# Optimization experiments

Hardware: AMD Instinct MI355X
Metric: run time of the kernel (lower is better)

## Reference

```python
import jax, jax.numpy as jnp
import numpy as np

S, T, B = 50, 50, 64
SRC_V, TRG_V = 36616, 23262
E, EH, DH = 300, 512, 1024


def setup_inputs() -> dict:
    key = jax.random.key(0)
    ks = jax.random.split(key, 20)
    n = lambda k, shape: jax.random.normal(k, shape, jnp.float32) * 0.05
    return {
        "train_src_batch": jax.random.randint(ks[0], (S, B), 0, SRC_V),
        "train_trg_batch": jax.random.randint(ks[1], (T, B), 0, TRG_V),
        "emb_en": n(ks[2], (SRC_V, E)),
        "emb_de": n(ks[3], (TRG_V, E)),
        "enc_W_ih_f": n(ks[4], (4 * EH, E)),
        "enc_W_hh_f": n(ks[5], (4 * EH, EH)),
        "enc_b_f": n(ks[6], (4 * EH,)),
        "enc_W_ih_b": n(ks[7], (4 * EH, E)),
        "enc_W_hh_b": n(ks[8], (4 * EH, EH)),
        "enc_b_b": n(ks[9], (4 * EH,)),
        "dec_W_ih": n(ks[10], (4 * DH, E + DH)),
        "dec_W_hh": n(ks[11], (4 * DH, DH)),
        "dec_b": n(ks[12], (4 * DH,)),
        "W_gen": n(ks[13], (TRG_V, DH)),
        "b_gen": n(ks[14], (TRG_V,)),
        "W_i": n(ks[15], (DH, DH)),
        "W_o": n(ks[16], (DH, 2 * DH)),
    }


def _lstm_step(x, h, c, W_ih, W_hh, b):
    # PyTorch gate order: i, f, g, o
    gates = x @ W_ih.T + h @ W_hh.T + b
    i, f, g, o = jnp.split(gates, 4, axis=-1)
    c_new = jax.nn.sigmoid(f) * c + jax.nn.sigmoid(i) * jnp.tanh(g)
    h_new = jax.nn.sigmoid(o) * jnp.tanh(c_new)
    return h_new, c_new


def _run_lstm(x_seq, W_ih, W_hh, b, hidden):
    h0 = jnp.zeros((x_seq.shape[1], hidden), x_seq.dtype)
    def step(carry, x):
        h, c = carry
        h, c = _lstm_step(x, h, c, W_ih, W_hh, b)
        return (h, c), h
    (h, c), hs = jax.lax.scan(step, (h0, h0), x_seq)
    return hs, h, c


def _forward(train_src_batch, train_trg_batch, emb_en, emb_de,
             enc_W_ih_f, enc_W_hh_f, enc_b_f, enc_W_ih_b, enc_W_hh_b, enc_b_b,
             dec_W_ih, dec_W_hh, dec_b, W_gen, b_gen, W_i, W_o):
    x = emb_en[train_src_batch]                       # [S,B,E]
    hs_f, hf, cf = _run_lstm(x, enc_W_ih_f, enc_W_hh_f, enc_b_f, EH)
    hs_b, hb, cb = _run_lstm(x[::-1], enc_W_ih_b, enc_W_hh_b, enc_b_b, EH)
    output_hs = jnp.concatenate([hs_f, hs_b[::-1]], axis=-1)  # [S,B,1024]
    # Faithful to h.contiguous().view(B,1024) on direction-major [2,B,512]
    h = jnp.reshape(jnp.stack([hf, hb], axis=0), (B, DH))
    c = jnp.reshape(jnp.stack([cf, cb], axis=0), (B, DH))

    emb_trg = emb_de[train_trg_batch[: T - 1]]        # [T-1,B,E]

    def step(carry, e):
        h, c = carry
        # score[j,b] = output_hs[j,b] . (W_i h[b])  (the diag of the original mm)
        scores = jnp.einsum('sbd,bd->sb', output_hs, h @ W_i.T)
        # legacy nn.Softmax() on 2D input -> softmax over dim=1 (batch axis)
        a = jax.nn.softmax(scores, axis=1)
        s_t = jnp.einsum('sb,sbd->bd', a, output_hs)
        c_t = jnp.tanh(jnp.concatenate([s_t, h], axis=1) @ W_o.T)
        dec_in = jnp.concatenate([c_t, e], axis=1)    # [B, 1024+300]
        h, c = _lstm_step(dec_in, h, c, dec_W_ih, dec_W_hh, dec_b)
        logp = jax.nn.log_softmax(h @ W_gen.T + b_gen, axis=1)
        return (h, c), logp

    _, outs = jax.lax.scan(step, (h, c), emb_trg)     # [T-1,B,V]
    out0 = jnp.zeros((1, B, TRG_V), outs.dtype)       # output[0] filled with 0
    return jnp.concatenate([out0, outs], axis=0)      # [T,B,V]


def reference(train_src_batch, train_trg_batch, emb_en, emb_de,
              enc_W_ih_f, enc_W_hh_f, enc_b_f, enc_W_ih_b, enc_W_hh_b, enc_b_b,
              dec_W_ih, dec_W_hh, dec_b, W_gen, b_gen, W_i, W_o):
    return _forward(train_src_batch, train_trg_batch, emb_en, emb_de,
                    enc_W_ih_f, enc_W_hh_f, enc_b_f, enc_W_ih_b, enc_W_hh_b, enc_b_b,
                    dec_W_ih, dec_W_hh, dec_b, W_gen, b_gen, W_i, W_o)
```

## Files before the change

kernel.cpp:

```cpp
#include <hip/hip_runtime.h>
#include <hip/hip_bf16.h>

#define SS 50
#define TT 50
#define BB 64
#define TRGV 23262
#define EE 300
#define EH 512
#define DH 1024

#define GMRE 3136
#define GMP 3200
#define GK 1024
#define GNRE TRGV
#define GNP 23296

typedef short bf16x8 __attribute__((ext_vector_type(8)));
typedef float f32x4 __attribute__((ext_vector_type(4)));

__device__ __forceinline__ void glds16(const void* g, void* l) {
  __builtin_amdgcn_global_load_lds(
      (const __attribute__((address_space(1))) void*)g,
      (__attribute__((address_space(3))) void*)l, 16, 0, 0);
}

__device__ __forceinline__ float sigm(float x) { return 1.f / (1.f + expf(-x)); }
__device__ __forceinline__ float sum4(f32x4 v) { return v[0] + v[1] + v[2] + v[3]; }
__device__ __forceinline__ float bfu2f(unsigned short u) {
  unsigned int x = ((unsigned)u) << 16;
  return __uint_as_float(x);
}

__device__ __forceinline__ void split2(float x, __hip_bfloat16& hi, __hip_bfloat16& lo) {
  hi = __float2bfloat16(x);
  lo = __float2bfloat16(x - __bfloat162float(hi));
}

__device__ __forceinline__ void gbarg(unsigned* arrive, unsigned* gen,
                                      int idxInGrp, int n, bool poller) {
  __syncthreads();
  unsigned g = __hip_atomic_load(gen, __ATOMIC_RELAXED, __HIP_MEMORY_SCOPE_AGENT);
  if (threadIdx.x == 0)
    __hip_atomic_store(arrive + idxInGrp * 16, g + 1u, __ATOMIC_RELEASE, __HIP_MEMORY_SCOPE_AGENT);
  if (poller) {
    int i = threadIdx.x;
    if (i < n) {
      while (__hip_atomic_load(arrive + i * 16, __ATOMIC_RELAXED, __HIP_MEMORY_SCOPE_AGENT) < g + 1u)
        __builtin_amdgcn_s_sleep(1);
      (void)__hip_atomic_load(arrive + i * 16, __ATOMIC_ACQUIRE, __HIP_MEMORY_SCOPE_AGENT);
    }
    __syncthreads();
    if (threadIdx.x == 0)
      __hip_atomic_store(gen, g + 1u, __ATOMIC_RELEASE, __HIP_MEMORY_SCOPE_AGENT);
  }
  if (threadIdx.x == 0) {
    while (__hip_atomic_load(gen, __ATOMIC_RELAXED, __HIP_MEMORY_SCOPE_AGENT) < g + 1u)
      __builtin_amdgcn_s_sleep(1);
    (void)__hip_atomic_load(gen, __ATOMIC_ACQUIRE, __HIP_MEMORY_SCOPE_AGENT);
  }
  __syncthreads();
}

__global__ void k_zero(float* __restrict__ p, long n) {
  long i = (long)blockIdx.x * 256 + threadIdx.x;
  if (i < n) p[i] = 0.f;
}
__global__ void k_zero_bf(__hip_bfloat16* __restrict__ p, long n) {
  long i = (long)blockIdx.x * 256 + threadIdx.x;
  if (i < n) p[i] = __float2bfloat16(0.f);
}

__global__ void k_embed(const int* __restrict__ src, const float* __restrict__ emb,
                        float* __restrict__ x) {
  int id = blockIdx.x * 256 + threadIdx.x;
  if (id >= SS * BB * EE) return;
  int sb = id / EE, e = id % EE;
  x[id] = emb[(long)src[sb] * EE + e];
}

__global__ void k_dbperm(const float* __restrict__ db, float* __restrict__ dbp) {
  int id = blockIdx.x * 256 + threadIdx.x;
  if (id >= 4096) return;
  int u = id >> 2, g = id & 3;
  dbp[id] = db[g * 1024 + u];
}

__global__ void k_split_pad(const float* __restrict__ in, int ld_in, int col_off,
                            int Kreal, int Kpad, int rows_real, long rows_pad,
                            int mode, __hip_bfloat16* __restrict__ out) {
  long id = (long)blockIdx.x * 256 + threadIdx.x;
  if (id >= rows_pad * Kpad) return;
  long r = id / Kpad;
  int k = id % Kpad;
  float v = 0.f;
  if (r < rows_real && k < Kreal) {
    if (mode == 3) {
      v = in[(long)k * ld_in + col_off + r];
    } else {
      long sr = r;
      if (mode == 1) sr = ((49 - (r >> 6)) << 6) + (r & 63);
      else if (mode == 2) sr = (long)(r & 3) * 1024 + (r >> 2);
      v = in[sr * ld_in + col_off + k];
    }
  }
  __hip_bfloat16 hi, lo;
  split2(v, hi, lo);
  out[r * 2 * Kpad + k] = hi;
  out[r * 2 * Kpad + Kpad + k] = lo;
}

__global__ void k_embgather_split(const int* __restrict__ trg, const float* __restrict__ emb,
                                  __hip_bfloat16* __restrict__ out) {
  long id = (long)blockIdx.x * 256 + threadIdx.x;
  if (id >= 3200L * 320) return;
  long r = id / 320;
  int k = id % 320;
  int t = r >> 6, b = r & 63;
  float v = 0.f;
  if (t < TT - 1 && k < EE) v = emb[(long)trg[t * BB + b] * EE + k];
  __hip_bfloat16 hi, lo;
  split2(v, hi, lo);
  out[r * 640 + k] = hi;
  out[r * 640 + 320 + k] = lo;
}

__global__ void k_tobf16_pad(const float* __restrict__ W, __hip_bfloat16* __restrict__ Wb,
                             long nrow_real, long nrow_pad, int K) {
  long id = (long)blockIdx.x * 256 + threadIdx.x;
  if (id >= nrow_pad * K) return;
  long r = id / K;
  Wb[id] = __float2bfloat16(r < nrow_real ? W[id] : 0.f);
}

__global__ void k_repackT(const float* __restrict__ in, __hip_bfloat16* __restrict__ out) {
  long id = (long)blockIdx.x * 256 + threadIdx.x;
  if (id >= 3200L * 1024) return;
  long r = id >> 10;
  int n = id & 1023;
  out[((long)(n >> 2) * 3200 + r) * 4 + (n & 3)] = __float2bfloat16(in[id]);
}

template<int OUTBF>
__global__ __launch_bounds__(256) void k_gsplit(
    const __hip_bfloat16* __restrict__ A2, const __hip_bfloat16* __restrict__ W2,
    const float* __restrict__ bias, void* __restrict__ Cout,
    int Mreal, int Nreal, int ldc, int Kpad) {
  __shared__ __hip_bfloat16 As[128 * 32];
  __shared__ __hip_bfloat16 Bs[128 * 32];
  int tid = threadIdx.x, lane = tid & 63, w = tid >> 6;
  long m0 = (long)blockIdx.y * 128, n0 = (long)blockIdx.x * 128;
  int lda2 = 2 * Kpad;
  int srow = lane >> 2;
  int scol = (lane & 3) * 8;
  char* lA0 = (char*)As + w * 2048;
  char* lA1 = lA0 + 1024;
  char* lB0 = (char*)Bs + w * 2048;
  char* lB1 = lB0 + 1024;
  int wm = (w >> 1) * 64, wn = (w & 1) * 64;
  int fr = lane & 15;
  int kc = (lane >> 4) * 8;
  f32x4 acc[4][4] = {};

  for (int seg = 0; seg < 3; ++seg) {
    const __hip_bfloat16* Ab = A2 + (seg == 1 ? Kpad : 0);
    const __hip_bfloat16* Wb = W2 + (seg == 2 ? Kpad : 0);
    const __hip_bfloat16* gA0 = Ab + (m0 + w * 32 + srow) * (long)lda2 + scol;
    const __hip_bfloat16* gA1 = gA0 + 16L * lda2;
    const __hip_bfloat16* gB0 = Wb + (n0 + w * 32 + srow) * (long)lda2 + scol;
    const __hip_bfloat16* gB1 = gB0 + 16L * lda2;
    for (int kt = 0; kt < Kpad / 32; ++kt) {
      int k0 = kt * 32;
      glds16(gA0 + k0, lA0);
      glds16(gA1 + k0, lA1);
      glds16(gB0 + k0, lB0);
      glds16(gB1 + k0, lB1);
      __syncthreads();
      bf16x8 a[4], b[4];
      for (int mi = 0; mi < 4; ++mi)
        a[mi] = *(const bf16x8*)(As + (wm + mi * 16 + fr) * 32 + kc);
      for (int ni = 0; ni < 4; ++ni)
        b[ni] = *(const bf16x8*)(Bs + (wn + ni * 16 + fr) * 32 + kc);
      for (int mi = 0; mi < 4; ++mi)
        for (int ni = 0; ni < 4; ++ni)
          acc[mi][ni] = __builtin_amdgcn_mfma_f32_16x16x32_bf16(a[mi], b[ni], acc[mi][ni], 0, 0, 0);
      __syncthreads();
    }
  }

  for (int mi = 0; mi < 4; ++mi) {
    for (int ni = 0; ni < 4; ++ni) {
      int n = (int)n0 + wn + ni * 16 + (lane & 15);
      if (n >= Nreal) continue;
      float bv = bias ? bias[n] : 0.f;
      for (int r = 0; r < 4; ++r) {
        int m = (int)m0 + wm + mi * 16 + (lane >> 4) * 4 + r;
        if (m >= Mreal) continue;
        float v = acc[mi][ni][r] + bv;
        if (OUTBF) ((__hip_bfloat16*)Cout)[(long)m * ldc + n] = __float2bfloat16(v);
        else ((float*)Cout)[(long)m * ldc + n] = v;
      }
    }
  }
}

__global__ __launch_bounds__(512) void persist_enc(
    const float* __restrict__ xW_f, const float* __restrict__ xW_b,
    const float* __restrict__ Whf, const float* __restrict__ Whb,
    float* __restrict__ hs, float* hA, float* hB, float* hA2, float* hB2,
    float* __restrict__ cf, float* __restrict__ cb,
    float* __restrict__ hd0, float* __restrict__ hT0, float* __restrict__ cdD,
    __hip_bfloat16* __restrict__ x2A, unsigned* __restrict__ bar) {
  __shared__ float WL[16 * 516];
  int t = threadIdx.x;
  int blk = blockIdx.x;
  int dir = blk >> 7, bl = blk & 127;
  const float* Whh = dir ? Whb : Whf;
  const float* xWb0 = dir ? xW_b : xW_f;
  float* c = dir ? cb : cf;
  float* hp = dir ? hA2 : hA;
  float* hn = dir ? hB2 : hB;
  unsigned* arrG = bar + dir * 2048;
  unsigned* genG = bar + 12288 + dir * 16;
  unsigned* arrA = bar + 4096;
  unsigned* genA = bar + 12320;

  for (int idx = t; idx < 16 * 512; idx += 512) {
    int r = idx >> 9, k = idx & 511;
    int srcrow = (r & 3) * 512 + (bl * 4 + (r >> 2));
    WL[r * 516 + k] = Whh[(long)srcrow * 512 + k];
  }
  __syncthreads();

  int j = t & 15;
  int b0 = t >> 4, b1 = b0 + 32;
  int g = j & 3;
  int ju = bl * 4 + (j >> 2);
  int lbase = (t & 63) & ~3;
  const f32x4* wq = (const f32x4*)(WL + j * 516);

  for (int s = 0; s < SS; ++s) {
    const f32x4* h0q = (const f32x4*)(hp + b0 * 512);
    const f32x4* h1q = (const f32x4*)(hp + b1 * 512);
    f32x4 v0 = {0, 0, 0, 0}, v1 = {0, 0, 0, 0};
    for (int q = 0; q < 128; ++q) {
      f32x4 wv = wq[q];
      v0 += wv * h0q[q];
      v1 += wv * h1q[q];
    }
    const float* xW = xWb0 + (long)(s * BB) * 2048;
    float a0 = sum4(v0) + xW[b0 * 2048 + g * 512 + ju];
    float a1 = sum4(v1) + xW[b1 * 2048 + g * 512 + ju];
    float gi0 = __shfl(a0, lbase + 0), gf0 = __shfl(a0, lbase + 1);
    float gg0 = __shfl(a0, lbase + 2), go0 = __shfl(a0, lbase + 3);
    float gi1 = __shfl(a1, lbase + 0), gf1 = __shfl(a1, lbase + 1);
    float gg1 = __shfl(a1, lbase + 2), go1 = __shfl(a1, lbase + 3);
    if ((t & 3) == 0) {
      int hscol = dir ? (512 + ju) : ju;
      int srow = dir ? (SS - 1 - s) : s;
      long hsrow0 = (long)(srow * BB + b0) * DH + hscol;
      long hsrow1 = (long)(srow * BB + b1) * DH + hscol;
      float cn0 = sigm(gf0) * c[b0 * 512 + ju] + sigm(gi0) * tanhf(gg0);
      float hn0 = sigm(go0) * tanhf(cn0);
      c[b0 * 512 + ju] = cn0;
      hn[b0 * 512 + ju] = hn0;
      hs[hsrow0] = hn0;
      float cn1 = sigm(gf1) * c[b1 * 512 + ju] + sigm(gi1) * tanhf(gg1);
      float hn1 = sigm(go1) * tanhf(cn1);
      c[b1 * 512 + ju] = cn1;
      hn[b1 * 512 + ju] = hn1;
      hs[hsrow1] = hn1;
    }
    float* tmp = hp; hp = hn; hn = tmp;
    gbarg(arrG, genG, bl, 128, bl == 0);
  }
  gbarg(arrA, genA, blk, 256, blk == 0);
  int gid = blk * 512 + t;
  if (gid < 65536) {
    int d2 = gid >> 15, b = (gid >> 9) & 63, j2 = gid & 511;
    float hv = (d2 ? hA2 : hA)[b * 512 + j2];
    float cv = (d2 ? cb : cf)[b * 512 + j2];
    hd0[gid] = hv;
    cdD[gid] = cv;
    int bp = gid >> 10, jp = gid & 1023;
    hT0[jp * 64 + bp] = hv;
    __hip_bfloat16 hi, lo;
    split2(hv, hi, lo);
    x2A[bp * 4096 + 1024 + jp] = hi;
    x2A[bp * 4096 + 3072 + jp] = lo;
  }
}

__global__ __launch_bounds__(1024) void persist_dec(
    const float* __restrict__ G, const __hip_bfloat16* __restrict__ HsWo1T,
    const float* __restrict__ Wo, const float* __restrict__ dWih,
    const float* __restrict__ dWhh, const __hip_bfloat16* __restrict__ Eg,
    float* __restrict__ h, float* __restrict__ hT,
    float* __restrict__ cd, float* __restrict__ scoresG,
    __hip_bfloat16* __restrict__ A_bf, __hip_bfloat16* __restrict__ x,
    float* __restrict__ gparts, unsigned* __restrict__ bar) {
  __shared__ __hip_bfloat16 WB[65536];
  __shared__ float Abuf[4096];
  int t = threadIdx.x;
  int blk = blockIdx.x;
  int w = t >> 6, lane = t & 63;
  unsigned* arrive = bar + 8192;
  unsigned* gen = bar + 12336;
  bool pol = (blk == 255);

  int nblk = blk >> 2, kchunk = blk & 3;

  for (int idx = t; idx < 64 * 512; idx += 1024) {
    int r = idx >> 9;
    int kk = idx & 511;
    int rp2 = nblk * 64 + r;
    long srcrow = (long)(rp2 & 3) * 1024 + (rp2 >> 2);
    int kabs = kchunk * 512 + kk;
    float v = (kabs < 1024) ? dWih[srcrow * 1324 + kabs]
                            : dWhh[srcrow * 1024 + (kabs - 1024)];
    __hip_bfloat16 hi, lo;
    split2(v, hi, lo);
    int c = kk >> 5, kq = (kk >> 3) & 3, e = kk & 7;
    int nt = r >> 4, rr = r & 15;
    WB[((((0 * 16 + c) * 4 + kq) * 4 + nt) * 16 + rr) * 8 + e] = hi;
    WB[((((1 * 16 + c) * 4 + kq) * 4 + nt) * 16 + rr) * 8 + e] = lo;
  }
  __syncthreads();

  int j = t & 15, b = t >> 4;
  int rp = blk * 16 + j;
  int nn = (blk & 3) * 16 + j;
  int ju = rp >> 2;
  int lbase = lane & ~3;
  const unsigned short* hwb = (const unsigned short*)HsWo1T + (long)blk * 3200 * 4;
  f32x4* Abuf4 = (f32x4*)Abuf;
  const float* wo2 = Wo + (long)(blk * 4) * 2048 + 1024;
  int mt = w & 3, nt = w >> 2;
  int row_a = mt * 16 + (lane & 15);
  int kq = lane >> 4;

  for (int ts = 0; ts < TT - 1; ++ts) {
    float eg = __bfloat162float(Eg[((long)(ts * BB + b)) * 4096 + rp]);

    if (blk < 200) {
      int s = blk >> 2;
      int bb = (blk & 3) * 16 + (t >> 6);
      int ln = t & 63;
      const f32x4* gq = (const f32x4*)(G + ((long)s * 64 + bb) * 1024);
      const f32x4* hq = (const f32x4*)(h + bb * 1024);
      f32x4 a4 = {0, 0, 0, 0};
      #pragma unroll
      for (int q = 0; q < 4; ++q) a4 += gq[ln + q * 64] * hq[ln + q * 64];
      float p = sum4(a4);
      for (int o = 1; o < 64; o <<= 1) p += __shfl_xor(p, o);
      if (ln == 0) scoresG[s * 64 + bb] = p;
    }
    {
      f32x4 z1 = {0, 0, 0, 0};
      for (int k = w * 64; k < w * 64 + 64; ++k) {
        float hb = hT[k * 64 + lane];
        f32x4 wv = {wo2[k], wo2[2048 + k], wo2[4096 + k], wo2[6144 + k]};
        z1 += hb * wv;
      }
      Abuf4[w * 64 + lane] = z1;
    }
    gbarg(arrive, gen, blk, 256, pol);

    {
      f32x4 z2 = {0, 0, 0, 0};
      for (int s = w; s < SS; s += 16) {
        float sc = scoresG[s * 64 + lane];
        float m = sc;
        for (int o = 32; o > 0; o >>= 1) m = fmaxf(m, __shfl_xor(m, o));
        float e = expf(sc - m);
        float su = e;
        for (int o = 32; o > 0; o >>= 1) su += __shfl_xor(su, o);
        const unsigned short* u4 = hwb + ((long)s * 64 + lane) * 4;
        f32x4 hv = {bfu2f(u4[0]), bfu2f(u4[1]), bfu2f(u4[2]), bfu2f(u4[3])};
        z2 += (e / su) * hv;
      }
      Abuf4[w * 64 + lane] += z2;
      __syncthreads();
      if (t < 256) {
        int bb = t >> 2, nl = t & 3;
        float sv = 0.f;
        for (int i = 0; i < 16; ++i) sv += Abuf[(i * 64 + bb) * 4 + nl];
        float ct = tanhf(sv);
        __hip_bfloat16 hi, lo;
        split2(ct, hi, lo);
        x[bb * 4096 + blk * 4 + nl] = hi;
        x[bb * 4096 + 2048 + blk * 4 + nl] = lo;
      }
    }
    gbarg(arrive, gen, blk, 256, pol);

    {
      f32x4 acc = {0, 0, 0, 0};
      const __hip_bfloat16* xrow = x + (long)row_a * 4096 + kchunk * 512 + kq * 8;
      #pragma unroll
      for (int pass = 0; pass < 3; ++pass) {
        int hh = (pass == 2) ? 1 : 0;
        int wh = (pass == 1) ? 1 : 0;
        const __hip_bfloat16* xp = xrow + hh * 2048;
        const __hip_bfloat16* wp = WB + (((wh * 16) * 4 + kq) * 4 + nt) * 16 * 8;
        #pragma unroll
        for (int c = 0; c < 16; ++c) {
          bf16x8 a = *(const bf16x8*)(xp + c * 32);
          bf16x8 bfr = *(const bf16x8*)(wp + (long)c * 4 * 4 * 16 * 8 + (lane & 15) * 8);
          acc = __builtin_amdgcn_mfma_f32_16x16x32_bf16(a, bfr, acc, 0, 0, 0);
        }
      }
      float* gp = gparts + (long)blk * 4096;
      for (int r = 0; r < 4; ++r) {
        int m = mt * 16 + kq * 4 + r;
        int n = nt * 16 + (lane & 15);
        gp[m * 64 + n] = acc[r];
      }
    }
    gbarg(arrive, gen, blk, 256, pol);

    {
      long gbase = (long)((blk >> 2) * 4) * 4096 + b * 64 + nn;
      float gv = gparts[gbase] + gparts[gbase + 4096] +
                 gparts[gbase + 2 * 4096] + gparts[gbase + 3 * 4096] + eg;
      float gi0 = __shfl(gv, lbase + 0), gf0 = __shfl(gv, lbase + 1);
      float gg0 = __shfl(gv, lbase + 2), go0 = __shfl(gv, lbase + 3);
      if ((t & 3) == 0) {
        float cn0 = sigm(gf0) * cd[b * DH + ju] + sigm(gi0) * tanhf(gg0);
        float hn0 = sigm(go0) * tanhf(cn0);
        cd[b * DH + ju] = cn0;
        h[b * DH + ju] = hn0;
        hT[ju * 64 + b] = hn0;
        __hip_bfloat16 hi, lo;
        split2(hn0, hi, lo);
        A_bf[(long)ts * (BB * DH) + b * DH + ju] = hi;
        x[b * 4096 + 1024 + ju] = hi;
        x[b * 4096 + 3072 + ju] = lo;
      }
    }
    gbarg(arrive, gen, blk, 256, pol);
  }
}

__global__ __launch_bounds__(256) void k_gen_mfma(
    const __hip_bfloat16* __restrict__ A, const __hip_bfloat16* __restrict__ Bw,
    const float* __restrict__ bias, float* __restrict__ C) {
  __shared__ __hip_bfloat16 As[128 * 32];
  __shared__ __hip_bfloat16 Bs[128 * 32];
  int tid = threadIdx.x;
  int lane = tid & 63, w = tid >> 6;
  long m0 = (long)blockIdx.y * 128, n0 = (long)blockIdx.x * 128;
  int srow = lane >> 2;
  int scol = (lane & 3) * 8;
  const __hip_bfloat16* gA0 = A + (m0 + w * 32 + srow) * GK + scol;
  const __hip_bfloat16* gA1 = gA0 + 16 * GK;
  const __hip_bfloat16* gB0 = Bw + (n0 + w * 32 + srow) * GK + scol;
  const __hip_bfloat16* gB1 = gB0 + 16 * GK;
  char* lA0 = (char*)As + w * 2048;
  char* lA1 = lA0 + 1024;
  char* lB0 = (char*)Bs + w * 2048;
  char* lB1 = lB0 + 1024;
  int wm = (w >> 1) * 64, wn = (w & 1) * 64;
  int fr = lane & 15;
  int kc = (lane >> 4) * 8;
  f32x4 acc[4][4] = {};
  for (int kt = 0; kt < GK / 32; ++kt) {
    int k0 = kt * 32;
    glds16(gA0 + k0, lA0);
    glds16(gA1 + k0, lA1);
    glds16(gB0 + k0, lB0);
    glds16(gB1 + k0, lB1);
    __syncthreads();
    bf16x8 a[4], b[4];
    for (int mi = 0; mi < 4; ++mi)
      a[mi] = *(const bf16x8*)(As + (wm + mi * 16 + fr) * 32 + kc);
    for (int ni = 0; ni < 4; ++ni)
      b[ni] = *(const bf16x8*)(Bs + (wn + ni * 16 + fr) * 32 + kc);
    for (int mi = 0; mi < 4; ++mi)
      for (int ni = 0; ni < 4; ++ni)
        acc[mi][ni] = __builtin_amdgcn_mfma_f32_16x16x32_bf16(a[mi], b[ni], acc[mi][ni], 0, 0, 0);
    __syncthreads();
  }
  for (int mi = 0; mi < 4; ++mi) {
    for (int ni = 0; ni < 4; ++ni) {
      int n = (int)n0 + wn + ni * 16 + (lane & 15);
      if (n >= GNRE) continue;
      float bv = bias[n];
      for (int r = 0; r < 4; ++r) {
        int m = (int)m0 + wm + mi * 16 + (lane >> 4) * 4 + r;
        if (m < GMRE) C[(long)m * TRGV + n] = acc[mi][ni][r] + bv;
      }
    }
  }
}

__global__ __launch_bounds__(256) void k_logsoftmax(float* __restrict__ out) {
  int r = blockIdx.x;
  float* p = out + (long)(BB + r) * TRGV;
  int tid = threadIdx.x;
  __shared__ float red[256];
  float m = -1e30f;
  for (int i = tid; i < TRGV; i += 256) m = fmaxf(m, p[i]);
  red[tid] = m;
  __syncthreads();
  for (int s = 128; s > 0; s >>= 1) {
    if (tid < s) red[tid] = fmaxf(red[tid], red[tid + s]);
    __syncthreads();
  }
  m = red[0];
  __syncthreads();
  float sum = 0.f;
  for (int i = tid; i < TRGV; i += 256) sum += expf(p[i] - m);
  red[tid] = sum;
  __syncthreads();
  for (int s = 128; s > 0; s >>= 1) {
    if (tid < s) red[tid] += red[tid + s];
    __syncthreads();
  }
  float lse = m + logf(red[0]);
  for (int i = tid; i < TRGV; i += 256) p[i] -= lse;
}

extern "C" void kernel_launch(void* const* d_in, const int* in_sizes, int n_in,
                              void* d_out, int out_size, void* d_ws, size_t ws_size,
                              hipStream_t stream) {
  const int* src = (const int*)d_in[0];
  const int* trg = (const int*)d_in[1];
  const float* emb_en = (const float*)d_in[2];
  const float* emb_de = (const float*)d_in[3];
  const float* eWih_f = (const float*)d_in[4];
  const float* eWhh_f = (const float*)d_in[5];
  const float* eb_f = (const float*)d_in[6];
  const float* eWih_b = (const float*)d_in[7];
  const float* eWhh_b = (const float*)d_in[8];
  const float* eb_b = (const float*)d_in[9];
  const float* dWih = (const float*)d_in[10];
  const float* dWhh = (const float*)d_in[11];
  const float* db = (const float*)d_in[12];
  const float* Wgen = (const float*)d_in[13];
  const float* bgen = (const float*)d_in[14];
  const float* Wi = (const float*)d_in[15];
  const float* Wo = (const float*)d_in[16];
  float* out = (float*)d_out;

  float* base = (float*)d_ws;
  __hip_bfloat16* xsf = (__hip_bfloat16*)base;
  __hip_bfloat16* xsb = (__hip_bfloat16*)(base + 1024000);
  __hip_bfloat16* Wihf2 = (__hip_bfloat16*)(base + 2048000);
  __hip_bfloat16* Wihb2 = (__hip_bfloat16*)(base + 2703360);
  float* xW_f = base + 3358720;
  float* xW_b = base + 9912320;
  __hip_bfloat16* hs2 = (__hip_bfloat16*)base;
  __hip_bfloat16* Wi2 = (__hip_bfloat16*)(base + 3276800);
  __hip_bfloat16* Wo12 = (__hip_bfloat16*)(base + 4325376);
  __hip_bfloat16* eg2 = (__hip_bfloat16*)(base + 5373952);
  __hip_bfloat16* Wce2 = (__hip_bfloat16*)(base + 6397952);
  __hip_bfloat16* E_g = (__hip_bfloat16*)(base + 7708672);
  __hip_bfloat16* Wgen_bf = (__hip_bfloat16*)base;
  float* p = base + 16465920;
  float* x_enc = p; p += SS * BB * EE;
  float* hs = p; p += (long)SS * BB * DH;
  float* G = p; p += (long)SS * BB * DH;
  float* HsWo1 = p; p += (long)SS * BB * DH;
  __hip_bfloat16* HsWo1T = (__hip_bfloat16*)p; p += (long)SS * BB * DH / 2;
  __hip_bfloat16* A_bf = (__hip_bfloat16*)p; p += (GMP * GK) / 2;
  __hip_bfloat16* x2A = (__hip_bfloat16*)p; p += (BB * 4096) / 2;
  float* gparts = p; p += 256 * 4096;
  float* dbp = p; p += 4096;
  float* scoresG = p; p += SS * BB;
  float* hd0 = p; p += BB * DH;
  float* hT0 = p; p += BB * DH;
  float* cd = p; p += BB * DH;
  float* hA = p; p += BB * EH;
  float* hB = p; p += BB * EH;
  float* hA2 = p; p += BB * EH;
  float* hB2 = p; p += BB * EH;
  float* cf = p; p += BB * EH;
  float* cb = p; p += BB * EH;
  unsigned* bar = (unsigned*)p; p += 12352;

  dim3 b256(256);

  k_embed<<<dim3((SS * BB * EE + 255) / 256), b256, 0, stream>>>(src, emb_en, x_enc);
  k_zero<<<dim3((6 * BB * EH + 255) / 256), b256, 0, stream>>>(hA, 6 * BB * EH);
  k_zero<<<dim3(49), b256, 0, stream>>>((float*)bar, 12352);
  k_zero<<<dim3((int)(((long)BB * TRGV + 255) / 256)), b256, 0, stream>>>(out, (long)BB * TRGV);
  k_zero_bf<<<dim3(((GMP - GMRE) * GK + 255) / 256), b256, 0, stream>>>(
      A_bf + (long)GMRE * GK, (long)(GMP - GMRE) * GK);
  k_dbperm<<<dim3(16), b256, 0, stream>>>(db, dbp);

  k_split_pad<<<dim3((3200 * 320 + 255) / 256), b256, 0, stream>>>(
      x_enc, EE, 0, EE, 320, 3200, 3200, 0, xsf);
  k_split_pad<<<dim3((3200 * 320 + 255) / 256), b256, 0, stream>>>(
      x_enc, EE, 0, EE, 320, 3200, 3200, 1, xsb);
  k_split_pad<<<dim3((2048 * 320 + 255) / 256), b256, 0, stream>>>(
      eWih_f, EE, 0, EE, 320, 2048, 2048, 0, Wihf2);
  k_split_pad<<<dim3((2048 * 320 + 255) / 256), b256, 0, stream>>>(
      eWih_b, EE, 0, EE, 320, 2048, 2048, 0, Wihb2);
  k_gsplit<0><<<dim3(16, 25), b256, 0, stream>>>(xsf, Wihf2, eb_f, xW_f, 3200, 2048, 2048, 320);
  k_gsplit<0><<<dim3(16, 25), b256, 0, stream>>>(xsb, Wihb2, eb_b, xW_b, 3200, 2048, 2048, 320);

  {
    void* args[] = {(void*)&xW_f, (void*)&xW_b, (void*)&eWhh_f, (void*)&eWhh_b,
                    (void*)&hs, (void*)&hA, (void*)&hB, (void*)&hA2, (void*)&hB2,
                    (void*)&cf, (void*)&cb, (void*)&hd0, (void*)&hT0, (void*)&cd,
                    (void*)&x2A, (void*)&bar};
    hipLaunchCooperativeKernel((const void*)persist_enc, dim3(256), dim3(512),
                               args, 0, stream);
  }

  k_split_pad<<<dim3((int)((3200L * 1024 + 255) / 256)), b256, 0, stream>>>(
      hs, DH, 0, DH, 1024, 3200, 3200, 0, hs2);
  k_split_pad<<<dim3((int)((1024L * 1024 + 255) / 256)), b256, 0, stream>>>(
      Wi, DH, 0, DH, 1024, 1024, 1024, 3, Wi2);
  k_split_pad<<<dim3((int)((1024L * 1024 + 255) / 256)), b256, 0, stream>>>(
      Wo, 2 * DH, 0, DH, 1024, 1024, 1024, 0, Wo12);
  k_embgather_split<<<dim3((int)((3200L * 320 + 255) / 256)), b256, 0, stream>>>(
      trg, emb_de, eg2);
  k_split_pad<<<dim3((int)((4096L * 320 + 255) / 256)), b256, 0, stream>>>(
      dWih, 1324, 1024, EE, 320, 4096, 4096, 2, Wce2);
  k_gsplit<0><<<dim3(8, 25), b256, 0, stream>>>(hs2, Wi2, (const float*)nullptr, G, 3200, 1024, 1024, 1024);
  k_gsplit<0><<<dim3(8, 25), b256, 0, stream>>>(hs2, Wo12, (const float*)nullptr, HsWo1, 3200, 1024, 1024, 1024);
  k_repackT<<<dim3((int)((3200L * 1024 + 255) / 256)), b256, 0, stream>>>(HsWo1, HsWo1T);
  k_gsplit<1><<<dim3(32, 25), b256, 0, stream>>>(eg2, Wce2, dbp, E_g, 3136, 4096, 4096, 320);

  {
    void* args[] = {(void*)&G, (void*)&HsWo1T, (void*)&Wo, (void*)&dWih, (void*)&dWhh,
                    (void*)&E_g, (void*)&hd0, (void*)&hT0, (void*)&cd, (void*)&scoresG,
                    (void*)&A_bf, (void*)&x2A, (void*)&gparts, (void*)&bar};
    hipLaunchCooperativeKernel((const void*)persist_dec, dim3(256), dim3(1024),
                               args, 0, stream);
  }

  k_tobf16_pad<<<dim3((int)(((long)GNP * GK + 255) / 256)), b256, 0, stream>>>(
      Wgen, Wgen_bf, GNRE, GNP, GK);
  k_gen_mfma<<<dim3(GNP / 128, GMP / 128), b256, 0, stream>>>(
      A_bf, Wgen_bf, bgen, out + (long)BB * TRGV);
  k_logsoftmax<<<dim3((TT - 1) * BB), b256, 0, stream>>>(out);
}
```

Baseline: 6.562 ms.

## Compute h·Wo2 with split-bf16 MFMA on idle decoder blocks

Replaces the per-block fp32 scalar loop that computed h times the second half of W_o (reading a transposed h copy and strided fp32 weights) with a 3-pass split-bf16 MFMA GEMM. It runs on 16 otherwise idle blocks (200-215) during the score phase and writes hWo2 to global memory, which the reducer then reads as its initial sum. This drops the hT transposed-state writes and moves the work off all 256 blocks. In exchange it adds a preprocessing split_pad pass for Wo22, an extra global buffer round-trip, and relies on the x bf16 hi/lo layout already holding h.

After: 10.43 ms. 58.9% more time.

```diff
diff --git a/kernel.cpp b/kernel.cpp
--- a/kernel.cpp
+++ b/kernel.cpp
@@ -208,7 +208,7 @@
     const float* __restrict__ Whf, const float* __restrict__ Whb,
     float* __restrict__ hs, float* hA, float* hB, float* hA2, float* hB2,
     float* __restrict__ cf, float* __restrict__ cb,
-    float* __restrict__ hd0, float* __restrict__ hT0, float* __restrict__ cdD,
+    float* __restrict__ hd0, float* __restrict__ cdD,
     __hip_bfloat16* __restrict__ x2A, unsigned* __restrict__ bar) {
   __shared__ float WL[16 * 516];
   int t = threadIdx.x;
@@ -282,7 +282,6 @@
     hd0[gid] = hv;
     cdD[gid] = cv;
     int bp = gid >> 10, jp = gid & 1023;
-    hT0[jp * 64 + bp] = hv;
     __hip_bfloat16 hi, lo;
     split2(hv, hi, lo);
     x2A[bp * 4096 + 1024 + jp] = hi;
@@ -292,9 +291,9 @@
 
 __global__ __launch_bounds__(1024) void persist_dec(
     const float* __restrict__ G, const __hip_bfloat16* __restrict__ HsWo1T,
-    const float* __restrict__ Wo, const float* __restrict__ dWih,
+    const __hip_bfloat16* __restrict__ Wo22, const float* __restrict__ dWih,
     const float* __restrict__ dWhh, const __hip_bfloat16* __restrict__ Eg,
-    float* __restrict__ h, float* __restrict__ hT,
+    float* __restrict__ h, float* __restrict__ hWo2,
     float* __restrict__ cd, float* __restrict__ scoresG,
     __hip_bfloat16* __restrict__ A_bf, __hip_bfloat16* __restrict__ x,
     float* __restrict__ gparts, unsigned* __restrict__ bar) {
@@ -333,7 +332,6 @@
   int lbase = lane & ~3;
   const unsigned short* hwb = (const unsigned short*)HsWo1T + (long)blk * 3200 * 4;
   f32x4* Abuf4 = (f32x4*)Abuf;
-  const float* wo2 = Wo + (long)(blk * 4) * 2048 + 1024;
   int mt = w & 3, nt = w >> 2;
   int row_a = mt * 16 + (lane & 15);
   int kq = lane >> 4;
@@ -353,15 +351,26 @@
       float p = sum4(a4);
       for (int o = 1; o < 64; o <<= 1) p += __shfl_xor(p, o);
       if (ln == 0) scoresG[s * 64 + bb] = p;
-    }
-    {
-      f32x4 z1 = {0, 0, 0, 0};
-      for (int k = w * 64; k < w * 64 + 64; ++k) {
-        float hb = hT[k * 64 + lane];
-        f32x4 wv = {wo2[k], wo2[2048 + k], wo2[4096 + k], wo2[6144 + k]};
-        z1 += hb * wv;
-      }
-      Abuf4[w * 64 + lane] = z1;
+    } else if (blk < 216) {
+      int n0 = (blk - 200) * 64;
+      int mi = w & 3, ni = w >> 2;
+      int fr = lane & 15, kq2 = lane >> 4;
+      const __hip_bfloat16* abase = x + (long)(mi * 16 + fr) * 4096 + kq2 * 8;
+      const __hip_bfloat16* bbase = Wo22 + (long)(n0 + ni * 16 + fr) * 2048 + kq2 * 8;
+      f32x4 acc = {0, 0, 0, 0};
+      #pragma unroll
+      for (int pass = 0; pass < 3; ++pass) {
+        int aoff = (pass == 1) ? 3072 : 1024;
+        int woff = (pass == 2) ? 1024 : 0;
+        #pragma unroll
+        for (int ks = 0; ks < 32; ++ks) {
+          bf16x8 a = *(const bf16x8*)(abase + aoff + ks * 32);
+          bf16x8 bfr = *(const bf16x8*)(bbase + woff + ks * 32);
+          acc = __builtin_amdgcn_mfma_f32_16x16x32_bf16(a, bfr, acc, 0, 0, 0);
+        }
+      }
+      for (int r = 0; r < 4; ++r)
+        hWo2[(mi * 16 + kq2 * 4 + r) * 1024 + n0 + ni * 16 + fr] = acc[r];
     }
     gbarg(arrive, gen, blk, 256, pol);
 
@@ -378,11 +387,11 @@
         f32x4 hv = {bfu2f(u4[0]), bfu2f(u4[1]), bfu2f(u4[2]), bfu2f(u4[3])};
         z2 += (e / su) * hv;
       }
-      Abuf4[w * 64 + lane] += z2;
+      Abuf4[w * 64 + lane] = z2;
       __syncthreads();
       if (t < 256) {
         int bb = t >> 2, nl = t & 3;
-        float sv = 0.f;
+        float sv = hWo2[bb * 1024 + blk * 4 + nl];
         for (int i = 0; i < 16; ++i) sv += Abuf[(i * 64 + bb) * 4 + nl];
         float ct = tanhf(sv);
         __hip_bfloat16 hi, lo;
@@ -429,7 +438,6 @@
         float hn0 = sigm(go0) * tanhf(cn0);
         cd[b * DH + ju] = cn0;
         h[b * DH + ju] = hn0;
-        hT[ju * 64 + b] = hn0;
         __hip_bfloat16 hi, lo;
         split2(hn0, hi, lo);
         A_bf[(long)ts * (BB * DH) + b * DH + ju] = hi;
@@ -562,13 +570,14 @@
   float* G = p; p += (long)SS * BB * DH;
   float* HsWo1 = p; p += (long)SS * BB * DH;
   __hip_bfloat16* HsWo1T = (__hip_bfloat16*)p; p += (long)SS * BB * DH / 2;
+  __hip_bfloat16* Wo22 = (__hip_bfloat16*)p; p += (long)DH * 2048 / 2;
   __hip_bfloat16* A_bf = (__hip_bfloat16*)p; p += (GMP * GK) / 2;
   __hip_bfloat16* x2A = (__hip_bfloat16*)p; p += (BB * 4096) / 2;
   float* gparts = p; p += 256 * 4096;
+  float* hWo2 = p; p += BB * DH;
   float* dbp = p; p += 4096;
   float* scoresG = p; p += SS * BB;
   float* hd0 = p; p += BB * DH;
-  float* hT0 = p; p += BB * DH;
   float* cd = p; p += BB * DH;
   float* hA = p; p += BB * EH;
   float* hB = p; p += BB * EH;
@@ -602,7 +611,7 @@
   {
     void* args[] = {(void*)&xW_f, (void*)&xW_b, (void*)&eWhh_f, (void*)&eWhh_b,
                     (void*)&hs, (void*)&hA, (void*)&hB, (void*)&hA2, (void*)&hB2,
-                    (void*)&cf, (void*)&cb, (void*)&hd0, (void*)&hT0, (void*)&cd,
+                    (void*)&cf, (void*)&cb, (void*)&hd0, (void*)&cd,
                     (void*)&x2A, (void*)&bar};
     hipLaunchCooperativeKernel((const void*)persist_enc, dim3(256), dim3(512),
                                args, 0, stream);
@@ -614,6 +623,8 @@
       Wi, DH, 0, DH, 1024, 1024, 1024, 3, Wi2);
   k_split_pad<<<dim3((int)((1024L * 1024 + 255) / 256)), b256, 0, stream>>>(
       Wo, 2 * DH, 0, DH, 1024, 1024, 1024, 0, Wo12);
+  k_split_pad<<<dim3((int)((1024L * 1024 + 255) / 256)), b256, 0, stream>>>(
+      Wo, 2 * DH, 1024, DH, 1024, 1024, 1024, 0, Wo22);
   k_embgather_split<<<dim3((int)((3200L * 320 + 255) / 256)), b256, 0, stream>>>(
       trg, emb_de, eg2);
   k_split_pad<<<dim3((int)((4096L * 320 + 255) / 256)), b256, 0, stream>>>(
@@ -624,8 +635,8 @@
   k_gsplit<1><<<dim3(32, 25), b256, 0, stream>>>(eg2, Wce2, dbp, E_g, 3136, 4096, 4096, 320);
 
   {
-    void* args[] = {(void*)&G, (void*)&HsWo1T, (void*)&Wo, (void*)&dWih, (void*)&dWhh,
-                    (void*)&E_g, (void*)&hd0, (void*)&hT0, (void*)&cd, (void*)&scoresG,
+    void* args[] = {(void*)&G, (void*)&HsWo1T, (void*)&Wo22, (void*)&dWih, (void*)&dWhh,
+                    (void*)&E_g, (void*)&hd0, (void*)&hWo2, (void*)&cd, (void*)&scoresG,
                     (void*)&A_bf, (void*)&x2A, (void*)&gparts, (void*)&bar};
     hipLaunchCooperativeKernel((const void*)persist_dec, dim3(256), dim3(1024),
                                args, 0, stream);
```
